# Performance work log

Measured on AMD Instinct MI355X. Metric: run time of the kernel, lower is better.

Reference implementation:

```python
import jax, jax.numpy as jnp
import numpy as np

_LOG_2PI = float(np.log(2.0 * np.pi))
N = 4096
N_VARS = 128
N_SOURCES = 8
_EPS = 1e-6


def setup_inputs() -> dict:
    key = jax.random.key(0)
    ks = jax.random.split(key, 6)
    data = jax.random.normal(ks[0], (N, N_VARS), dtype=jnp.float32)
    sources = jax.random.randint(ks[1], (N,), 0, N_SOURCES, dtype=jnp.int32)
    miss_mask = jax.random.bernoulli(ks[2], 0.3, (N, N_VARS))
    # Strictly lower-triangular DAG weights, small spectral norm so I - W is well conditioned
    W_eff = jnp.tril(jax.random.normal(ks[3], (N_VARS, N_VARS), dtype=jnp.float32) * 0.05, k=-1)
    log_sigma2 = jnp.zeros((N_SOURCES, N_VARS), dtype=jnp.float32)
    mu = jnp.zeros((N_VARS,), dtype=jnp.float32)
    sample_weights = jax.random.uniform(ks[4], (N,), dtype=jnp.float32)
    return {"data": data, "W_eff": W_eff, "log_sigma2": log_sigma2, "mu": mu,
            "sample_weights": sample_weights, "sources": sources, "miss_mask": miss_mask}


def reference(data, W_eff, log_sigma2, mu, sample_weights, sources, miss_mask):
    # Gaussian log-likelihood over observed entries only, per sample.
    # Original torch code loops over unique (source, missingness-pattern) groups and
    # does a Cholesky of the observed sub-covariance Sigma_oo + eps*I.  We compute the
    # mathematically identical quantity fully batched via the masked-covariance trick:
    #   Sigma_tilde = M (Sigma + eps I) M + diag(1 - obs)
    # whose logdet equals logdet(Sigma_oo + eps I_oo) and whose quadratic form on the
    # zero-filled centred data equals x_o^T (Sigma_oo + eps I)^{-1} x_o.
    D = data.shape[1]
    I = jnp.eye(D, dtype=data.dtype)
    T = jnp.linalg.solve(I - W_eff, I)                       # [D, D]
    sigma2 = jnp.maximum(jnp.exp(log_sigma2), _EPS)          # [S, D]
    # Sigma_s = T^T diag(sigma2_s) T for every source
    Sigma = jnp.einsum('ij,si,ik->sjk', T, sigma2, T)        # [S, D, D]

    obs = (~miss_mask).astype(data.dtype)                    # [N, D]
    xc = (data - mu[None, :]) * obs                          # centred, zero at missing

    Sig_i = Sigma[sources] + _EPS * I                        # [N, D, D]
    M = obs[:, :, None] * obs[:, None, :]                    # [N, D, D] obs outer obs
    Sig_t = Sig_i * M + I * (1.0 - obs)[:, None, :]          # identity on missing coords

    L = jnp.linalg.cholesky(Sig_t)                           # [N, D, D]
    z = jax.scipy.linalg.solve_triangular(L, xc[:, :, None], lower=True)[:, :, 0]
    quad = jnp.sum(z * z, axis=1)                            # [N]
    logdet = 2.0 * jnp.sum(jnp.log(jnp.diagonal(L, axis1=1, axis2=2)), axis=1)
    d_obs = jnp.sum(obs, axis=1)                             # [N]
    ll = -0.5 * (quad + logdet + d_obs * _LOG_2PI)           # [N]
    return jnp.sum(ll * sample_weights)
```

## Files before the change

### kernel.cpp

```cpp
#include <hip/hip_runtime.h>
#include <math.h>

#define DD 128
#define NSRC 8
#define EMAX 32
#define MFAST 62
#define LOG_2PI 1.83787706640934548356f
#define LN2F 0.69314718055994531f
#define EPSF 1e-6f

__device__ inline int tri_row_of(int e) {
    float f = sqrtf(8.f * (float)e + 1.f);
    int r = (int)((f - 1.f) * 0.5f);
    if ((r + 1) * (r + 2) / 2 <= e) ++r;
    else if (r * (r + 1) / 2 > e) --r;
    return r;
}

__global__ __launch_bounds__(128) void k_precompute(
    const float* __restrict__ W, const float* __restrict__ ls2,
    const unsigned int* __restrict__ mw, int n_words,
    float* __restrict__ Q, float* __restrict__ ldS,
    int* __restrict__ flagarr, float* __restrict__ partial,
    int* __restrict__ ovf_cnt)
{
    __shared__ float Bs[DD][DD + 1];
    __shared__ float r[4][DD + 1];
    __shared__ float sinv[DD];
    __shared__ float part2[2];
    __shared__ int fsh[2];
    const int tid = threadIdx.x;
    const int s   = blockIdx.x >> 5;
    const int i0  = (blockIdx.x & 31) * 4;

    if (blockIdx.x == 0) {
        if (tid < 64)  partial[tid] = 0.f;
        if (tid == 64) *ovf_cnt = 0;
    }

    int gid = (blockIdx.x * 128 + tid) * 4;
    int f = 0;
    #pragma unroll
    for (int t = 0; t < 4; ++t) {
        int idx = gid + t;
        if (idx < n_words) {
            unsigned int v = mw[idx];
            if (v > 1u) f |= 1;
            if (v == 0x3F800000u) f |= 2;
        }
    }
    unsigned long long bA = __ballot(f & 1);
    unsigned long long bB = __ballot(f & 2);
    if ((tid & 63) == 0) fsh[tid >> 6] = (bA ? 1 : 0) | (bB ? 2 : 0);

    const float4* __restrict__ W4 = (const float4*)W;
    #pragma unroll 8
    for (int idx = tid; idx < (DD * DD) / 4; idx += 128) {
        float4 w = W4[idx];
        int row = idx >> 5;
        int col = (idx & 31) << 2;
        Bs[row][col + 0] = ((col + 0) == row ? 1.f : 0.f) - w.x;
        Bs[row][col + 1] = ((col + 1) == row ? 1.f : 0.f) - w.y;
        Bs[row][col + 2] = ((col + 2) == row ? 1.f : 0.f) - w.z;
        Bs[row][col + 3] = ((col + 3) == row ? 1.f : 0.f) - w.w;
    }
    sinv[tid] = 1.f / fmaxf(expf(ls2[s * DD + tid]), EPSF);
    __syncthreads();
    if (tid == 0) flagarr[blockIdx.x] = fsh[0] | fsh[1];
    for (int a = 0; a < 4; ++a)
        r[a][tid] = Bs[i0 + a][tid] * sinv[tid];
    __syncthreads();

    const int j = tid;
    float acc0 = 0.f, acc1 = 0.f, acc2 = 0.f, acc3 = 0.f;
    #pragma unroll 8
    for (int d = 0; d < DD; ++d) {
        float bj = Bs[j][d];
        acc0 += r[0][d] * bj;
        acc1 += r[1][d] * bj;
        acc2 += r[2][d] * bj;
        acc3 += r[3][d] * bj;
    }
    size_t base = ((size_t)s * DD + i0) * DD + j;
    Q[base         ] = acc0;
    Q[base +     DD] = acc1;
    Q[base + 2 * DD] = acc2;
    Q[base + 3 * DD] = acc3;

    if (i0 == 0) {
        float v = logf(fmaxf(expf(ls2[s * DD + tid]), EPSF));
        for (int o = 32; o; o >>= 1) v += __shfl_down(v, o, 64);
        if ((tid & 63) == 0) part2[tid >> 6] = v;
        __syncthreads();
        if (tid == 0) ldS[s] = part2[0] + part2[1];
    }
}

#define CHOL_STEP(CR, CW)                                                     \
    {                                                                         \
        float dk   = CR[kk];                                                  \
        float invd = __builtin_amdgcn_rcpf(dk);                               \
        logacc += __log2f(dk);                                                \
        const unsigned b1 = (unsigned)(kk + 1) << 8;                          \
        const int rem = m - kk;                                               \
        const int nT  = (((rem * (rem + 1)) >> 1) + 63) >> 6;                 \
        _Pragma("unroll")                                                     \
        for (int t = 0; t < EMAX; ++t) {                                      \
            if (t >= nT) break;                     \
            const unsigned k2 = key[t];                                       \
            const bool alive = (k2 >= b1);                                    \
            const int air = alive ? (int)(k2 & 255u) : 63;                    \
            const int ajc = alive ? (int)(k2 >> 8)   : 63;                    \
            float ci = CR[air];                                               \
            float cj = CR[ajc];                                               \
            val[t] -= ci * cj * invd;         \
            if (k2 - b1 < 256u) CW[k2 & 255u] = val[t];                       \
        }                                                                     \
    }

__global__ __launch_bounds__(64) void k_fast(
    const float* __restrict__ data, const float* __restrict__ mu,
    const float* __restrict__ wgt, const int* __restrict__ src,
    const void* __restrict__ miss, const int* __restrict__ flagarr,
    const float* __restrict__ Q, const float* __restrict__ ldS,
    float* __restrict__ partial, int* __restrict__ ovf_cnt,
    int* __restrict__ ovf_list)
{
    __shared__ float xsh[DD];
    __shared__ float ysh[DD];
    __shared__ int   midx[64];
    __shared__ float csc0[64];
    __shared__ float csc1[64];

    const int i = blockIdx.x, lane = threadIdx.x;
    const int s = src[i];
    const float* Qs = Q + (size_t)s * DD * DD;
    const size_t base = (size_t)i * DD;
    const int j0 = 2 * lane, j1 = 2 * lane + 1;

    int fl = 0;
    #pragma unroll
    for (int t = 0; t < 4; ++t) fl |= flagarr[lane + 64 * t];
    unsigned long long fb1 = __ballot(fl & 1);
    unsigned long long fb2 = __ballot(fl & 2);
    const int f = (fb1 ? 1 : 0) | (fb2 ? 2 : 0);

    bool mmE, mmO;
    if (f & 2) {
        const float* M = (const float*)miss;
        mmE = M[base + j0] != 0.f;  mmO = M[base + j1] != 0.f;
    } else if (f & 1) {
        const unsigned char* M = (const unsigned char*)miss;
        mmE = M[base + j0] != 0;    mmO = M[base + j1] != 0;
    } else {
        const int* M = (const int*)miss;
        mmE = M[base + j0] != 0;    mmO = M[base + j1] != 0;
    }

    unsigned long long bE = __ballot(mmE), bO = __ballot(mmO);
    const int m = __popcll(bE) + __popcll(bO);
    if (m > MFAST) {
        if (lane == 0) { int pos = atomicAdd(ovf_cnt, 1); ovf_list[pos] = i; }
        return;
    }
    unsigned long long lt = (1ull << lane) - 1ull;
    if (mmE) midx[__popcll(bE & lt)] = j0;
    if (mmO) midx[__popcll(bE) + __popcll(bO & lt)] = j1;

    float x0 = mmE ? 0.f : (data[base + j0] - mu[j0]);
    float x1 = mmO ? 0.f : (data[base + j1] - mu[j1]);
    xsh[j0] = x0;
    xsh[j1] = x1;
    if (lane == 63) { csc0[63] = 0.f; csc1[63] = 0.f; }
    __syncthreads();

    float y0 = 0.f, y1 = 0.f, z0 = 0.f, z1 = 0.f;
    #pragma unroll 8
    for (int k = 0; k < DD; k += 2) {
        float xk0 = xsh[k], xk1 = xsh[k + 1];
        float2 qa = *(const float2*)(Qs + (size_t)k * DD + j0);
        float2 qb = *(const float2*)(Qs + (size_t)(k + 1) * DD + j0);
        y0 += xk0 * qa.x;  y1 += xk0 * qa.y;
        z0 += xk1 * qb.x;  z1 += xk1 * qb.y;
    }
    y0 += z0;  y1 += z1;
    ysh[j0] = y0;
    ysh[j1] = y1;
    float p = x0 * y0 + x1 * y1;
    for (int o = 32; o; o >>= 1) p += __shfl_down(p, o, 64);
    __syncthreads();

    const int cntT = ((m + 1) * (m + 2)) >> 1;
    unsigned key[EMAX];
    float    val[EMAX];
    #pragma unroll
    for (int t = 0; t < EMAX; ++t) {
        key[t] = 0u; val[t] = 0.f;
        int e = lane + (t << 6);
        if (e < cntT) {
            int q  = tri_row_of(e);
            int jc = m - q;
            int ir = jc + (e - ((q * (q + 1)) >> 1));
            float v;
            if (ir == m) {
                v = (jc == m) ? 0.f : ysh[midx[jc]];
            } else {
                v = Qs[(size_t)(midx[ir] * DD + midx[jc])];
            }
            key[t] = ((unsigned)jc << 8) | (unsigned)ir;
            val[t] = v;
            if (jc == 0) csc0[ir] = v;
        }
    }
    __syncthreads();

    float logacc = 0.f;
    {
        int kk = 0;
        while (kk < m) {
            CHOL_STEP(csc0, csc1)
            ++kk;
            if (kk >= m) break;
            CHOL_STEP(csc1, csc0)
            ++kk;
        }
    }

    if (lane == 0) {
        float ll = -0.5f * ((p + val[0]) + logacc * LN2F + ldS[s]
                            + (float)(DD - m) * LOG_2PI);
        atomicAdd(&partial[i & 63], ll * wgt[i]);
    }
}

__global__ __launch_bounds__(128) void k_tail(
    const float* __restrict__ data, const float* __restrict__ mu,
    const float* __restrict__ wgt, const int* __restrict__ src,
    const void* __restrict__ miss, const int* __restrict__ flagarr,
    const float* __restrict__ Q, const float* __restrict__ ldS,
    float* __restrict__ partial, const int* __restrict__ ovf_cnt,
    const int* __restrict__ ovf_list, float* __restrict__ out)
{
    __shared__ __align__(16) float xsh[DD];
    __shared__ float ysh[DD];
    __shared__ int   midx[DD];
    __shared__ float cscv[DD + 1];
    __shared__ float tri[(DD + 1) * (DD + 2) / 2];
    __shared__ float bc[2];
    __shared__ float red[2];
    __shared__ int   sh_m;
    __shared__ int   sh_f;

    const int tid = threadIdx.x;
    if (tid == 0) sh_f = 0;
    __syncthreads();
    {
        int fl = flagarr[tid] | flagarr[tid + 128];
        if (fl) atomicOr(&sh_f, fl);
    }
    __syncthreads();
    const int f = sh_f;

    const int novf = *ovf_cnt;
    for (int j = 0; j < novf; ++j) {
        const int i = ovf_list[j];
        if (tid == 0) sh_m = 0;
        __syncthreads();

        const int s = src[i];
        const float* Qs = Q + (size_t)s * DD * DD;
        const size_t g = (size_t)i * DD + tid;
        bool mm;
        if (f & 2)      mm = ((const float*)miss)[g] != 0.f;
        else if (f & 1) mm = ((const unsigned char*)miss)[g] != 0;
        else            mm = ((const int*)miss)[g] != 0;

        float xv = mm ? 0.f : (data[g] - mu[tid]);
        xsh[tid] = xv;
        if (mm) { int pos = atomicAdd(&sh_m, 1); midx[pos] = tid; }
        __syncthreads();
        const int m = sh_m;

        const float4* qrow = (const float4*)(Qs + (size_t)tid * DD);
        const float4* x4   = (const float4*)xsh;
        float acc = 0.f;
        #pragma unroll 8
        for (int d = 0; d < DD / 4; ++d) {
            float4 q = qrow[d], xx = x4[d];
            acc += q.x * xx.x + q.y * xx.y + q.z * xx.z + q.w * xx.w;
        }
        ysh[tid] = acc;
        float pp = xv * acc;
        for (int o = 32; o; o >>= 1) pp += __shfl_down(pp, o, 64);
        if ((tid & 63) == 0) red[tid >> 6] = pp;
        __syncthreads();

        const int cntA = (m * (m + 1)) >> 1;
        for (int e = tid; e < cntA; e += 128) {
            int a = tri_row_of(e);
            int b = e - ((a * (a + 1)) >> 1);
            tri[e] = Qs[(size_t)midx[a] * DD + midx[b]];
        }
        for (int b = tid; b < m; b += 128) tri[cntA + b] = ysh[midx[b]];
        if (tid == 0) tri[cntA + m] = 0.f;
        __syncthreads();

        float logacc = 0.f;
        if (m > 0) {
            if (tid == 0) {
                float d0 = tri[0];
                bc[1] = d0;
                float sq = sqrtf(d0);
                bc[0] = 1.f / sq;
                tri[0] = sq;
            }
            __syncthreads();
            for (int k = 0; k < m; ++k) {
                float inv = bc[0];
                if (tid == 0) logacc += logf(bc[1]);
                for (int ii = k + 1 + tid; ii <= m; ii += 128) {
                    int off = (ii * (ii + 1)) >> 1;
                    float v = tri[off + k] * inv;
                    tri[off + k] = v;
                    cscv[ii] = v;
                }
                __syncthreads();
                int qn  = m - k;
                int cnt = (qn * (qn + 1)) >> 1;
                for (int e = tid; e < cnt; e += 128) {
                    int ri = tri_row_of(e);
                    int rj = e - ((ri * (ri + 1)) >> 1);
                    int ii = k + 1 + ri, jj = k + 1 + rj;
                    int off = (ii * (ii + 1)) >> 1;
                    float v = tri[off + jj] - cscv[ii] * cscv[jj];
                    if (ii == jj && jj == k + 1 && k + 1 < m) {
                        bc[1] = v;
                        float sq = sqrtf(v);
                        bc[0] = 1.f / sq;
                        tri[off + jj] = sq;
                    } else {
                        tri[off + jj] = v;
                    }
                }
                __syncthreads();
            }
        }

        if (tid == 0) {
            float quad2 = (m > 0) ? -tri[cntA + m] : 0.f;
            float quad1 = red[0] + red[1];
            float ll = -0.5f * ((quad1 - quad2) + logacc + ldS[s]
                                + (float)(DD - m) * LOG_2PI);
            atomicAdd(&partial[i & 63], ll * wgt[i]);
        }
        __syncthreads();
    }

    __syncthreads();
    if (tid < 64) {
        float v = partial[tid];
        for (int o = 32; o; o >>= 1) v += __shfl_down(v, o, 64);
        if (tid == 0) out[0] = v;
    }
}

extern "C" void kernel_launch(void* const* d_in, const int* in_sizes, int n_in,
                              void* d_out, int out_size, void* d_ws, size_t ws_size,
                              hipStream_t stream)
{
    const float* data = (const float*)d_in[0];
    const float* W    = (const float*)d_in[1];
    const float* ls2  = (const float*)d_in[2];
    const float* mu   = (const float*)d_in[3];
    const float* wgt  = (const float*)d_in[4];
    const int*   src  = (const int*)d_in[5];
    const void*  miss = (const void*)d_in[6];
    float* out = (float*)d_out;

    float* Q        = (float*)d_ws;
    float* ldS      = Q + (size_t)NSRC * DD * DD;
    float* partial  = ldS + NSRC;
    int*   flagarr  = (int*)(partial + 64);
    int*   ovf_cnt  = flagarr + 256;
    int*   ovf_list = ovf_cnt + 1;

    const int n       = in_sizes[0] / DD;
    const int n_words = (n * DD) / 4;

    hipLaunchKernelGGL(k_precompute, dim3(NSRC * 32), dim3(128), 0, stream,
                       W, ls2, (const unsigned int*)miss, n_words,
                       Q, ldS, flagarr, partial, ovf_cnt);
    hipLaunchKernelGGL(k_fast, dim3(n), dim3(64), 0, stream,
                       data, mu, wgt, src, miss, flagarr, Q, ldS,
                       partial, ovf_cnt, ovf_list);
    hipLaunchKernelGGL(k_tail, dim3(1), dim3(128), 0, stream,
                       data, mu, wgt, src, miss, flagarr, Q, ldS,
                       partial, ovf_cnt, ovf_list, out);
}
```

Measured before the change: 161.4 us.

## Process two Cholesky columns per step in fast per-sample kernel

Restructures the per-sample Cholesky elimination so that each step eliminates two pivots at once, applying a rank-2 update from two column buffers and double-buffering four shared column arrays. This halves the number of sequential elimination steps and their shared-memory column exchanges. The inner loop now exits through a wave-wide __any check instead of a computed tile count, and each step adds a __syncthreads. The cost is more shared loads and arithmetic per step, plus a separate final single-column step when the count is odd.

```diff
diff --git a/kernel.cpp b/kernel.cpp
--- a/kernel.cpp
+++ b/kernel.cpp
@@ -96,25 +96,55 @@
     }
 }
 
-#define CHOL_STEP(CR, CW)                                                     \
+#define CHOL_PAIR(CR0, CR1, CW0, CW1)                                         \
+    {                                                                         \
+        float d0   = CR0[kk];                                                 \
+        float t10  = CR0[kk + 1];                                             \
+        float d1r  = CR1[kk + 1];                                             \
+        float inv0 = __builtin_amdgcn_rcpf(d0);                               \
+        float g    = t10 * inv0;                                              \
+        float d1   = d1r - t10 * g;                                           \
+        float inv1 = __builtin_amdgcn_rcpf(d1);                               \
+        logacc += __log2f(d0) + __log2f(d1);                                  \
+        const unsigned b1 = (unsigned)(kk + 1) << 8;                          \
+        const unsigned b2 = (unsigned)(kk + 2) << 8;                          \
+        const unsigned b3 = (unsigned)(kk + 3) << 8;                          \
+        _Pragma("unroll")                                                     \
+        for (int t = 0; t < EMAX; ++t) {                                      \
+            bool alive = (key[t] >= b1);                                      \
+            if (!__any(alive)) break;                                         \
+            if (alive) {                                                      \
+                int ir = (int)(key[t] & 255u);                                \
+                int jc = (int)(key[t] >> 8);                                  \
+                float ci0 = CR0[ir];                                          \
+                float cj0 = CR0[jc];                                          \
+                float ci1 = CR1[ir];                                          \
+                float cj1 = CR1[jc];                                          \
+                float pi1 = ci1 - g * ci0;                                    \
+                float pj1 = cj1 - g * cj0;                                    \
+                val[t] -= ci0 * cj0 * inv0 + pi1 * pj1 * inv1;                \
+                if (key[t] - b2 < 256u) CW0[ir] = val[t];                     \
+                if (key[t] - b3 < 256u) CW1[ir] = val[t];                     \
+            }                                                                 \
+        }                                                                     \
+        __syncthreads();                                                      \
+    }
+
+#define CHOL_FINAL(CR)                                                        \
     {                                                                         \
         float dk   = CR[kk];                                                  \
         float invd = __builtin_amdgcn_rcpf(dk);                               \
         logacc += __log2f(dk);                                                \
         const unsigned b1 = (unsigned)(kk + 1) << 8;                          \
-        const int rem = m - kk;                                               \
-        const int nT  = (((rem * (rem + 1)) >> 1) + 63) >> 6;                 \
         _Pragma("unroll")                                                     \
         for (int t = 0; t < EMAX; ++t) {                                      \
-            if (t >= nT) break;                     \
-            const unsigned k2 = key[t];                                       \
-            const bool alive = (k2 >= b1);                                    \
-            const int air = alive ? (int)(k2 & 255u) : 63;                    \
-            const int ajc = alive ? (int)(k2 >> 8)   : 63;                    \
-            float ci = CR[air];                                               \
-            float cj = CR[ajc];                                               \
-            val[t] -= ci * cj * invd;         \
-            if (k2 - b1 < 256u) CW[k2 & 255u] = val[t];                       \
+            bool alive = (key[t] >= b1);                                      \
+            if (!__any(alive)) break;                                         \
+            if (alive) {                                                      \
+                int ir = (int)(key[t] & 255u);                                \
+                int jc = (int)(key[t] >> 8);                                  \
+                val[t] -= CR[ir] * CR[jc] * invd;                             \
+            }                                                                 \
         }                                                                     \
     }
 
@@ -129,8 +159,10 @@
     __shared__ float xsh[DD];
     __shared__ float ysh[DD];
     __shared__ int   midx[64];
-    __shared__ float csc0[64];
-    __shared__ float csc1[64];
+    __shared__ float cA0[64];
+    __shared__ float cA1[64];
+    __shared__ float cB0[64];
+    __shared__ float cB1[64];
 
     const int i = blockIdx.x, lane = threadIdx.x;
     const int s = src[i];
@@ -171,7 +203,6 @@
     float x1 = mmO ? 0.f : (data[base + j1] - mu[j1]);
     xsh[j0] = x0;
     xsh[j1] = x1;
-    if (lane == 63) { csc0[63] = 0.f; csc1[63] = 0.f; }
     __syncthreads();
 
     float y0 = 0.f, y1 = 0.f, z0 = 0.f, z1 = 0.f;
@@ -209,21 +240,24 @@
             }
             key[t] = ((unsigned)jc << 8) | (unsigned)ir;
             val[t] = v;
-            if (jc == 0) csc0[ir] = v;
+            if (jc == 0)      cA0[ir] = v;
+            else if (jc == 1) cA1[ir] = v;
         }
     }
     __syncthreads();
 
     float logacc = 0.f;
-    {
-        int kk = 0;
-        while (kk < m) {
-            CHOL_STEP(csc0, csc1)
-            ++kk;
-            if (kk >= m) break;
-            CHOL_STEP(csc1, csc0)
-            ++kk;
-        }
+    int kk = 0;
+    while (kk + 1 < m) {
+        CHOL_PAIR(cA0, cA1, cB0, cB1)
+        kk += 2;
+        if (kk + 1 >= m) break;
+        CHOL_PAIR(cB0, cB1, cA0, cA1)
+        kk += 2;
+    }
+    if (kk < m) {
+        if ((kk >> 1) & 1) { CHOL_FINAL(cB0) }
+        else               { CHOL_FINAL(cA0) }
     }
 
     if (lane == 0) {
```

After: 196.8 us. 21.9% more time.
